# Kernel optimization log

Hardware: AMD Instinct MI355X
Metric: run time of the kernel (lower is better)

The kernel has to match this reference:

```python
import jax, jax.numpy as jnp
import numpy as np

H = 256        # hidden_dim
GD = 16        # genome_dim
GL = 16        # genome_len
L = 2          # n_layers
NH = 4         # n_heads
ED = 256       # embed_dim (of generated network)
CS = 256       # chunk_size (== H so chunk feedback into GRU is well-formed)
TOTAL = 4 * ED * ED + 4 * ED          # 263168
NCH = (TOTAL + CS - 1) // CS          # 1028 sequential GRU steps
B = 16


def setup_inputs() -> dict:
    key = jax.random.key(0)
    ks = iter(jax.random.split(key, 32))
    def p(shape, s=0.02):
        return jax.random.normal(next(ks), shape, jnp.float32) * s
    return dict(
        genome_seq=jax.random.normal(next(ks), (B, GL, GD), jnp.float32),
        embed_W=p((H, GD)), embed_b=jnp.zeros((H,), jnp.float32),
        qkv_W=p((L, 3 * H, H)), qkv_b=jnp.zeros((L, 3 * H), jnp.float32),
        attn_out_W=p((L, H, H)), attn_out_b=jnp.zeros((L, H), jnp.float32),
        ln1_g=jnp.ones((L, H), jnp.float32), ln1_b=jnp.zeros((L, H), jnp.float32),
        ln2_g=jnp.ones((L, H), jnp.float32), ln2_b=jnp.zeros((L, H), jnp.float32),
        ffn_W1=p((L, 4 * H, H)), ffn_b1=jnp.zeros((L, 4 * H), jnp.float32),
        ffn_W2=p((L, H, 4 * H)), ffn_b2=jnp.zeros((L, H), jnp.float32),
        gru_Wih=p((3 * H, H)), gru_Whh=p((3 * H, H)),
        gru_bih=jnp.zeros((3 * H,), jnp.float32), gru_bhh=jnp.zeros((3 * H,), jnp.float32),
        out_W=p((CS, H)), out_b=jnp.zeros((CS,), jnp.float32),
    )


def _ln(x, g, b, eps=1e-5):
    m = x.mean(-1, keepdims=True)
    v = ((x - m) ** 2).mean(-1, keepdims=True)
    return (x - m) / jnp.sqrt(v + eps) * g + b


def reference(genome_seq, embed_W, embed_b, qkv_W, qkv_b, attn_out_W, attn_out_b,
              ln1_g, ln1_b, ln2_g, ln2_b, ffn_W1, ffn_b1, ffn_W2, ffn_b2,
              gru_Wih, gru_Whh, gru_bih, gru_bhh, out_W, out_b):
    b = genome_seq.shape[0]
    dh = H // NH
    scale = 1.0 / np.sqrt(dh).astype(np.float32)

    h = genome_seq @ embed_W.T + embed_b                      # [B, S, H]
    # post-norm transformer encoder, relu FFN (PyTorch defaults, no dropout)
    for l in range(L):
        qkv = h @ qkv_W[l].T + qkv_b[l]                        # [B, S, 3H]
        q, k, v = jnp.split(qkv, 3, axis=-1)
        q = q.reshape(b, GL, NH, dh)
        k = k.reshape(b, GL, NH, dh)
        v = v.reshape(b, GL, NH, dh)
        scores = jnp.einsum('bshd,bthd->bhst', q, k) * scale
        attn = jax.nn.softmax(scores, axis=-1)
        o = jnp.einsum('bhst,bthd->bshd', attn, v).reshape(b, GL, H)
        h = _ln(h + o @ attn_out_W[l].T + attn_out_b[l], ln1_g[l], ln1_b[l])
        f = jax.nn.relu(h @ ffn_W1[l].T + ffn_b1[l]) @ ffn_W2[l].T + ffn_b2[l]
        h = _ln(h + f, ln2_g[l], ln2_b[l])

    latent = h.mean(axis=1)                                    # [B, H]

    # sequential chunk generation: 1 GRU step + Linear per chunk, fed back
    def step(carry, _):
        x, hid = carry
        gi = x @ gru_Wih.T + gru_bih
        gh = hid @ gru_Whh.T + gru_bhh
        ir, iz, inn = jnp.split(gi, 3, axis=-1)
        hr, hz, hn = jnp.split(gh, 3, axis=-1)
        r = jax.nn.sigmoid(ir + hr)
        z = jax.nn.sigmoid(iz + hz)
        n = jnp.tanh(inn + r * hn)
        hid = (1.0 - z) * n + z * hid
        chunk = hid @ out_W.T + out_b                          # [B, CS]
        return (chunk, hid), chunk

    h0 = jnp.zeros((b, H), latent.dtype)
    _, chunks = jax.lax.scan(step, (latent, h0), None, length=NCH)  # [NCH, B, CS]
    flat = jnp.moveaxis(chunks, 0, 1).reshape(b, NCH * CS)
    return flat[:, :TOTAL]
```

## Files before the change

### kernel.cpp

```cpp
#include <hip/hip_runtime.h>


typedef unsigned int uint_t;
typedef int v4i __attribute__((ext_vector_type(4)));

static constexpr size_t WS_HB   = 0;
static constexpr size_t WS_QKV  = 65536;
static constexpr size_t WS_AO   = 262144;
static constexpr size_t WS_F1   = 327680;
static constexpr size_t WS_LAT  = 589824;
static constexpr size_t WS_GI0  = 593920;
static constexpr size_t WS_CV   = 606208;
static constexpr size_t WS_MS   = 607232;
static constexpr size_t WS_M8   = 608256;
static constexpr size_t WS_HSEQ = 673792;

__device__ inline float sigf(float x){
    return __builtin_amdgcn_rcpf(1.0f + __builtin_amdgcn_exp2f(-1.442695041f*x));
}
__device__ inline float tanh_fast(float x){
    return 1.0f - 2.0f*__builtin_amdgcn_rcpf(1.0f + __builtin_amdgcn_exp2f(2.885390082f*x));
}


__global__ __launch_bounds__(256) void k_embed(const float* gs, const float* eW,
                                               const float* eb, float* ws){
    int bs = blockIdx.x;
    int i  = threadIdx.x;
    const float* g = gs + bs*16;
    float acc = eb[i];
#pragma unroll
    for(int d=0; d<16; ++d) acc += g[d]*eW[i*16+d];
    ws[WS_HB + (size_t)bs*256 + i] = acc;
}

__global__ __launch_bounds__(256) void k_qkv(const float* qkvW, const float* qkvb,
                                             float* ws, int l){
    __shared__ float hr[16][256];
    int b = blockIdx.x, jc = blockIdx.y;
    for(int idx=threadIdx.x; idx<4096; idx+=256)
        hr[idx>>8][idx&255] = ws[WS_HB + (size_t)(b*16+(idx>>8))*256 + (idx&255)];
    __syncthreads();
    int j = jc*256 + threadIdx.x;
    float bias = qkvb[l*768 + j];
    float acc[16];
#pragma unroll
    for(int s=0;s<16;++s) acc[s]=bias;
    const float* wr = qkvW + (size_t)(l*768 + j)*256;
    for(int k=0;k<256;k+=4){
        float4 w4 = *(const float4*)(wr+k);
#pragma unroll
        for(int s=0;s<16;++s)
            acc[s] += w4.x*hr[s][k] + w4.y*hr[s][k+1] + w4.z*hr[s][k+2] + w4.w*hr[s][k+3];
    }
    for(int s=0;s<16;++s) ws[WS_QKV + (size_t)(b*16+s)*768 + j] = acc[s];
}

__global__ __launch_bounds__(256) void k_attn(float* ws){
    __shared__ float ql[16][64], kl[16][64], vl[16][64], sc[16][16];
    int b = blockIdx.x>>2, hh = blockIdx.x&3;
    for(int idx=threadIdx.x; idx<1024; idx+=256){
        int s_=idx>>6, d=idx&63;
        const float* base = &ws[WS_QKV + (size_t)(b*16+s_)*768 + hh*64 + d];
        ql[s_][d]=base[0]; kl[s_][d]=base[256]; vl[s_][d]=base[512];
    }
    __syncthreads();
    int s = threadIdx.x>>4, t = threadIdx.x&15;
    float a=0.f;
#pragma unroll
    for(int d=0; d<64; ++d) a += ql[s][d]*kl[t][d];
    sc[s][t] = a*0.125f;
    __syncthreads();
    if(threadIdx.x<16){
        int r=threadIdx.x;
        float m=-1e30f;
#pragma unroll
        for(int tt=0;tt<16;++tt) m=fmaxf(m,sc[r][tt]);
        float e[16]; float sum=0.f;
#pragma unroll
        for(int tt=0;tt<16;++tt){ e[tt]=__expf(sc[r][tt]-m); sum+=e[tt]; }
        float inv=1.0f/sum;
#pragma unroll
        for(int tt=0;tt<16;++tt) sc[r][tt]=e[tt]*inv;
    }
    __syncthreads();
    int dg = (threadIdx.x&15)*4;
#pragma unroll
    for(int dd=0;dd<4;++dd){
        int d = dg+dd; float o=0.f;
#pragma unroll
        for(int tt=0;tt<16;++tt) o += sc[s][tt]*vl[tt][d];
        ws[WS_AO + (size_t)(b*16+s)*256 + hh*64 + d] = o;
    }
}

__global__ __launch_bounds__(256) void k_ao_ln(const float* aoW, const float* aob,
                                               const float* g1, const float* b1,
                                               float* ws, int l){
    __shared__ float ao[256]; __shared__ float red[256];
    int bs = blockIdx.x, i = threadIdx.x;
    ao[i] = ws[WS_AO + (size_t)bs*256 + i];
    __syncthreads();
    const float* wr = aoW + (size_t)(l*256+i)*256;
    float acc = aob[l*256+i];
    for(int k=0;k<256;k+=4){
        float4 w4 = *(const float4*)(wr+k);
        acc += w4.x*ao[k]+w4.y*ao[k+1]+w4.z*ao[k+2]+w4.w*ao[k+3];
    }
    float x = ws[WS_HB + (size_t)bs*256 + i] + acc;
    red[i]=x; __syncthreads();
    for(int off=128;off>0;off>>=1){ if(i<off) red[i]+=red[i+off]; __syncthreads(); }
    float m = red[0]*(1.0f/256.0f); __syncthreads();
    float d = x-m;
    red[i]=d*d; __syncthreads();
    for(int off=128;off>0;off>>=1){ if(i<off) red[i]+=red[i+off]; __syncthreads(); }
    float v = red[0]*(1.0f/256.0f);
    float y = d / sqrtf(v+1e-5f);
    ws[WS_HB + (size_t)bs*256 + i] = y*g1[l*256+i] + b1[l*256+i];
}

__global__ __launch_bounds__(256) void k_ffn1(const float* W1, const float* fb1,
                                              float* ws, int l){
    __shared__ float hr[16][256];
    int b = blockIdx.x, jc = blockIdx.y;
    for(int idx=threadIdx.x; idx<4096; idx+=256)
        hr[idx>>8][idx&255] = ws[WS_HB + (size_t)(b*16+(idx>>8))*256 + (idx&255)];
    __syncthreads();
    int j = jc*256 + threadIdx.x;
    float bias = fb1[l*1024+j];
    float acc[16];
#pragma unroll
    for(int s=0;s<16;++s) acc[s]=bias;
    const float* wr = W1 + (size_t)(l*1024+j)*256;
    for(int k=0;k<256;k+=4){
        float4 w4 = *(const float4*)(wr+k);
#pragma unroll
        for(int s=0;s<16;++s)
            acc[s] += w4.x*hr[s][k] + w4.y*hr[s][k+1] + w4.z*hr[s][k+2] + w4.w*hr[s][k+3];
    }
    for(int s=0;s<16;++s)
        ws[WS_F1 + (size_t)(b*16+s)*1024 + j] = fmaxf(acc[s],0.0f);
}

__global__ __launch_bounds__(256) void k_ffn2_ln(const float* W2, const float* fb2,
                                                 const float* g2, const float* b2v,
                                                 float* ws, int l){
    __shared__ float f1r[1024]; __shared__ float red[256];
    int bs = blockIdx.x, i = threadIdx.x;
    for(int idx=i; idx<1024; idx+=256) f1r[idx] = ws[WS_F1 + (size_t)bs*1024 + idx];
    __syncthreads();
    const float* wr = W2 + (size_t)(l*256+i)*1024;
    float acc = fb2[l*256+i];
    for(int k=0;k<1024;k+=4){
        float4 w4 = *(const float4*)(wr+k);
        acc += w4.x*f1r[k]+w4.y*f1r[k+1]+w4.z*f1r[k+2]+w4.w*f1r[k+3];
    }
    float x = ws[WS_HB + (size_t)bs*256 + i] + acc;
    red[i]=x; __syncthreads();
    for(int off=128;off>0;off>>=1){ if(i<off) red[i]+=red[i+off]; __syncthreads(); }
    float m = red[0]*(1.0f/256.0f); __syncthreads();
    float d = x-m;
    red[i]=d*d; __syncthreads();
    for(int off=128;off>0;off>>=1){ if(i<off) red[i]+=red[i+off]; __syncthreads(); }
    float v = red[0]*(1.0f/256.0f);
    float y = d / sqrtf(v+1e-5f);
    ws[WS_HB + (size_t)bs*256 + i] = y*g2[l*256+i] + b2v[l*256+i];
}

__global__ __launch_bounds__(256) void k_latent(float* ws){
    int b=blockIdx.x, i=threadIdx.x; float a=0.f;
#pragma unroll
    for(int s=0;s<16;++s) a += ws[WS_HB + (size_t)(b*16+s)*256 + i];
    ws[WS_LAT + (size_t)b*256 + i] = a*(1.0f/16.0f);
}


__global__ __launch_bounds__(768) void k_gi0(const float* Wih, const float* bih,
                                             float* ws){
    __shared__ float lat[256];
    int b=blockIdx.x, j=threadIdx.x;
    if(j<256) lat[j]=ws[WS_LAT + (size_t)b*256 + j];
    __syncthreads();
    const float* wr = Wih + (size_t)j*256;
    float acc = bih[j];
    for(int k=0;k<256;k+=4){
        float4 w4=*(const float4*)(wr+k);
        acc += w4.x*lat[k]+w4.y*lat[k+1]+w4.z*lat[k+2]+w4.w*lat[k+3];
    }
    ws[WS_GI0 + (size_t)b*768 + j] = acc;
}

__global__ __launch_bounds__(256) void k_prepm(const float* Wih, const float* Whh,
                                               const float* bih, const float* bhh,
                                               const float* outW, const float* outb,
                                               float* ws){
    __shared__ float wrow[256]; __shared__ float red[256];
    __shared__ signed char q8[256];
    int r=blockIdx.x, c=threadIdx.x;
    bool hasA = (r<768);
    wrow[c] = hasA ? Wih[(size_t)r*256+c] : 0.0f;
    __syncthreads();
    float m;
    if(hasA){
        float a=0.f;
        for(int k=0;k<256;++k) a += wrow[k]*outW[(size_t)k*256+c];
        if(r<512) a += Whh[(size_t)r*256+c];
        m=a;
    } else {
        m = Whh[(size_t)(r-256)*256+c];
    }
    red[c] = wrow[c]*outb[c];
    __syncthreads();
    for(int off=128;off>0;off>>=1){ if(c<off) red[c]+=red[c+off]; __syncthreads(); }
    if(c==0){
        float cv;
        if(r<512)       cv = red[0] + bih[r] + bhh[r];
        else if(r<768)  cv = red[0] + bih[r];
        else            cv = bhh[r-256];
        ws[WS_CV + r] = cv;
    }
    __syncthreads();
    red[c] = fabsf(m);
    __syncthreads();
    for(int off=128;off>0;off>>=1){ if(c<off) red[c]=fmaxf(red[c],red[c+off]); __syncthreads(); }
    float rowmax = red[0];
    float inv = rowmax>0.f ? 127.0f/rowmax : 0.0f;
    q8[c] = (signed char)__float2int_rn(m*inv);
    if(c==0) ws[WS_MS + r] = rowmax>0.f ? rowmax*(1.0f/(127.0f*127.0f)) : 0.0f;
    __syncthreads();
    if(c<64){
        uint_t u = ((uint_t)(unsigned char)q8[4*c  ])
                 | ((uint_t)(unsigned char)q8[4*c+1] << 8)
                 | ((uint_t)(unsigned char)q8[4*c+2] << 16)
                 | ((uint_t)(unsigned char)q8[4*c+3] << 24);
        ((uint_t*)ws)[WS_M8 + (size_t)r*64 + c] = u;
    }
}


__global__ __launch_bounds__(512,2) void k_chain(const float* bhh, float* ws){
    __shared__ alignas(16) signed char h8[2][256];
    int tid = threadIdx.x;
    int b   = blockIdx.x;
    int l   = tid & 63;
    int w   = tid >> 6;
    int col = l & 15;
    int grp = l >> 4;
    int g0  = w*32 + col;

    const uint_t* Mdw = (const uint_t*)ws + WS_M8;

    v4i wf[8][4];
    float C8[8], MS8[8];
#pragma unroll
    for(int s=0;s<4;++s){
#pragma unroll
        for(int half=0; half<2; ++half){
            int f = s*2 + half;
            int row = s*256 + w*32 + half*16 + col;
            const uint_t* src = Mdw + (size_t)row*64 + grp*4;
#pragma unroll
            for(int kt=0;kt<4;++kt)
                wf[f][kt] = *(const v4i*)(src + kt*16);
            C8[f]  = ws[WS_CV + row];
            MS8[f] = ws[WS_MS + row];
        }
    }

    const float* gi = ws + WS_GI0 + (size_t)b*768;
    int g1 = g0 + 16;
    float r0 = sigf(gi[g0]     + bhh[g0]);
    float z0 = sigf(gi[256+g0] + bhh[256+g0]);
    float n0 = tanh_fast(gi[512+g0] + r0*bhh[512+g0]);
    float hp0 = (1.0f-z0)*n0;
    float r1 = sigf(gi[g1]     + bhh[g1]);
    float z1 = sigf(gi[256+g1] + bhh[256+g1]);
    float n1 = tanh_fast(gi[512+g1] + r1*bhh[512+g1]);
    float hp1 = (1.0f-z1)*n1;

    float* hsp = ws + WS_HSEQ + (size_t)b*256;
    if(grp < 2){
        float v = grp ? hp1 : hp0;
        h8[0][w*32 + (l&31)] = (signed char)__float2int_rn(v*127.0f);
        hsp[w*32 + (l&31)] = v;
    }
    asm volatile("s_waitcnt lgkmcnt(0)" ::: "memory");
    __builtin_amdgcn_s_barrier();
    asm volatile("" ::: "memory");

    const v4i vzero = {0,0,0,0};
    int po = 0;
    for(int t=1; t<1028; ++t){
        hsp += 4096;
        v4i af[4];
#pragma unroll
        for(int kt=0;kt<4;++kt)
            af[kt] = *(const v4i*)&h8[po][kt*64 + grp*16];
        v4i acc[8];
#pragma unroll
        for(int f=0;f<8;++f){
            acc[f] = __builtin_amdgcn_mfma_i32_16x16x64_i8(af[0], wf[f][0], vzero, 0,0,0);
#pragma unroll
            for(int kt=1;kt<4;++kt)
                acc[f] = __builtin_amdgcn_mfma_i32_16x16x64_i8(af[kt], wf[f][kt], acc[f], 0,0,0);
        }
        float yr0 = MS8[0]*(float)acc[0][0] + C8[0];
        float yr1 = MS8[1]*(float)acc[1][0] + C8[1];
        float yz0 = MS8[2]*(float)acc[2][0] + C8[2];
        float yz1 = MS8[3]*(float)acc[3][0] + C8[3];
        float yn0 = MS8[4]*(float)acc[4][0] + C8[4];
        float yn1 = MS8[5]*(float)acc[5][0] + C8[5];
        float yh0 = MS8[6]*(float)acc[6][0] + C8[6];
        float yh1 = MS8[7]*(float)acc[7][0] + C8[7];
        float rr0 = sigf(yr0), rr1 = sigf(yr1);
        float zz0 = sigf(yz0), zz1 = sigf(yz1);
        float nn0 = tanh_fast(yn0 + rr0*yh0);
        float nn1 = tanh_fast(yn1 + rr1*yh1);
        hp0 = (1.0f-zz0)*nn0 + zz0*hp0;
        hp1 = (1.0f-zz1)*nn1 + zz1*hp1;
        if(grp < 2){
            float v = grp ? hp1 : hp0;
            h8[po^1][w*32 + (l&31)] = (signed char)__float2int_rn(v*127.0f);
            hsp[w*32 + (l&31)] = v;
        }
        asm volatile("s_waitcnt lgkmcnt(0)" ::: "memory");
        __builtin_amdgcn_s_barrier();
        asm volatile("" ::: "memory");
        po ^= 1;
    }
}

__global__ __launch_bounds__(256) void k_epi(const float* outW, const float* outb,
                                             const float* ws, float* out){
    __shared__ float ht[16][256];
    int t = blockIdx.x, j = threadIdx.x;
    for(int idx=j; idx<4096; idx+=256)
        ht[idx>>8][idx&255] = ws[WS_HSEQ + (size_t)t*4096 + idx];
    __syncthreads();
    const float* wr = outW + (size_t)j*256;
    float bias = outb[j];
    float acc[16];
#pragma unroll
    for(int bb=0;bb<16;++bb) acc[bb]=bias;
    for(int k=0;k<256;k+=4){
        float4 w4 = *(const float4*)(wr+k);
#pragma unroll
        for(int bb=0;bb<16;++bb)
            acc[bb] += w4.x*ht[bb][k]+w4.y*ht[bb][k+1]+w4.z*ht[bb][k+2]+w4.w*ht[bb][k+3];
    }
#pragma unroll
    for(int bb=0;bb<16;++bb)
        out[(size_t)bb*263168 + (size_t)t*256 + j] = acc[bb];
}


extern "C" void kernel_launch(void* const* d_in, const int* in_sizes, int n_in,
                              void* d_out, int out_size, void* d_ws, size_t ws_size,
                              hipStream_t stream){
    const float* gs   = (const float*)d_in[0];
    const float* eW   = (const float*)d_in[1];
    const float* eb   = (const float*)d_in[2];
    const float* qkvW = (const float*)d_in[3];
    const float* qkvb = (const float*)d_in[4];
    const float* aoW  = (const float*)d_in[5];
    const float* aob  = (const float*)d_in[6];
    const float* g1   = (const float*)d_in[7];
    const float* b1   = (const float*)d_in[8];
    const float* g2   = (const float*)d_in[9];
    const float* b2   = (const float*)d_in[10];
    const float* W1   = (const float*)d_in[11];
    const float* fb1  = (const float*)d_in[12];
    const float* W2   = (const float*)d_in[13];
    const float* fb2  = (const float*)d_in[14];
    const float* Wih  = (const float*)d_in[15];
    const float* Whh  = (const float*)d_in[16];
    const float* bih  = (const float*)d_in[17];
    const float* bhh  = (const float*)d_in[18];
    const float* outW = (const float*)d_in[19];
    const float* outb = (const float*)d_in[20];
    float* ws  = (float*)d_ws;
    float* out = (float*)d_out;

    k_embed<<<256,256,0,stream>>>(gs,eW,eb,ws);
    for(int l=0;l<2;++l){
        k_qkv    <<<dim3(16,3),256,0,stream>>>(qkvW,qkvb,ws,l);
        k_attn   <<<64,256,0,stream>>>(ws);
        k_ao_ln  <<<256,256,0,stream>>>(aoW,aob,g1,b1,ws,l);
        k_ffn1   <<<dim3(16,4),256,0,stream>>>(W1,fb1,ws,l);
        k_ffn2_ln<<<256,256,0,stream>>>(W2,fb2,g2,b2,ws,l);
    }
    k_latent<<<16,256,0,stream>>>(ws);
    k_gi0   <<<16,768,0,stream>>>(Wih,bih,ws);
    k_prepm <<<1024,256,0,stream>>>(Wih,Whh,bih,bhh,outW,outb,ws);
    k_chain <<<16,512,0,stream>>>(bhh,ws);
    k_epi   <<<1028,256,0,stream>>>(outW,outb,ws,out);
}
```

Before: 1.127 ms.

## Fuse transformer stages into fewer kernels and halve per-lane GRU gate work

Merges embedding with the weight-prep kernel, fuses QKV projection with attention per batch-head, and fuses attention-out, LayerNorm, FFN1 and FFN2 with a second LayerNorm into one kernel per token. The latent mean is also folded into the gi0 kernel. Together this cuts the launch count from about 16 to 7 and removes intermediate global round-trips. In the GRU chain kernel each lane now handles one hidden unit, picked by lane parity, instead of computing two and discarding one, which shortens the serial per-step gate math. The cost is that the fused FFN kernel has every one of 256 blocks re-read the full W1 matrix, with less parallelism per weight row.

Result: faster. 1.096 ms (-2.7%).

```diff
diff --git a/kernel.cpp b/kernel.cpp
--- a/kernel.cpp
+++ b/kernel.cpp
@@ -5,10 +5,7 @@
 typedef int v4i __attribute__((ext_vector_type(4)));
 
 static constexpr size_t WS_HB   = 0;
-static constexpr size_t WS_QKV  = 65536;
 static constexpr size_t WS_AO   = 262144;
-static constexpr size_t WS_F1   = 327680;
-static constexpr size_t WS_LAT  = 589824;
 static constexpr size_t WS_GI0  = 593920;
 static constexpr size_t WS_CV   = 606208;
 static constexpr size_t WS_MS   = 607232;
@@ -23,180 +20,26 @@
 }
 
 
-__global__ __launch_bounds__(256) void k_embed(const float* gs, const float* eW,
-                                               const float* eb, float* ws){
-    int bs = blockIdx.x;
-    int i  = threadIdx.x;
-    const float* g = gs + bs*16;
-    float acc = eb[i];
-#pragma unroll
-    for(int d=0; d<16; ++d) acc += g[d]*eW[i*16+d];
-    ws[WS_HB + (size_t)bs*256 + i] = acc;
-}
-
-__global__ __launch_bounds__(256) void k_qkv(const float* qkvW, const float* qkvb,
-                                             float* ws, int l){
-    __shared__ float hr[16][256];
-    int b = blockIdx.x, jc = blockIdx.y;
-    for(int idx=threadIdx.x; idx<4096; idx+=256)
-        hr[idx>>8][idx&255] = ws[WS_HB + (size_t)(b*16+(idx>>8))*256 + (idx&255)];
-    __syncthreads();
-    int j = jc*256 + threadIdx.x;
-    float bias = qkvb[l*768 + j];
-    float acc[16];
-#pragma unroll
-    for(int s=0;s<16;++s) acc[s]=bias;
-    const float* wr = qkvW + (size_t)(l*768 + j)*256;
-    for(int k=0;k<256;k+=4){
-        float4 w4 = *(const float4*)(wr+k);
-#pragma unroll
-        for(int s=0;s<16;++s)
-            acc[s] += w4.x*hr[s][k] + w4.y*hr[s][k+1] + w4.z*hr[s][k+2] + w4.w*hr[s][k+3];
-    }
-    for(int s=0;s<16;++s) ws[WS_QKV + (size_t)(b*16+s)*768 + j] = acc[s];
-}
-
-__global__ __launch_bounds__(256) void k_attn(float* ws){
-    __shared__ float ql[16][64], kl[16][64], vl[16][64], sc[16][16];
-    int b = blockIdx.x>>2, hh = blockIdx.x&3;
-    for(int idx=threadIdx.x; idx<1024; idx+=256){
-        int s_=idx>>6, d=idx&63;
-        const float* base = &ws[WS_QKV + (size_t)(b*16+s_)*768 + hh*64 + d];
-        ql[s_][d]=base[0]; kl[s_][d]=base[256]; vl[s_][d]=base[512];
-    }
-    __syncthreads();
-    int s = threadIdx.x>>4, t = threadIdx.x&15;
-    float a=0.f;
-#pragma unroll
-    for(int d=0; d<64; ++d) a += ql[s][d]*kl[t][d];
-    sc[s][t] = a*0.125f;
-    __syncthreads();
-    if(threadIdx.x<16){
-        int r=threadIdx.x;
-        float m=-1e30f;
-#pragma unroll
-        for(int tt=0;tt<16;++tt) m=fmaxf(m,sc[r][tt]);
-        float e[16]; float sum=0.f;
-#pragma unroll
-        for(int tt=0;tt<16;++tt){ e[tt]=__expf(sc[r][tt]-m); sum+=e[tt]; }
-        float inv=1.0f/sum;
-#pragma unroll
-        for(int tt=0;tt<16;++tt) sc[r][tt]=e[tt]*inv;
-    }
-    __syncthreads();
-    int dg = (threadIdx.x&15)*4;
-#pragma unroll
-    for(int dd=0;dd<4;++dd){
-        int d = dg+dd; float o=0.f;
-#pragma unroll
-        for(int tt=0;tt<16;++tt) o += sc[s][tt]*vl[tt][d];
-        ws[WS_AO + (size_t)(b*16+s)*256 + hh*64 + d] = o;
-    }
-}
-
-__global__ __launch_bounds__(256) void k_ao_ln(const float* aoW, const float* aob,
-                                               const float* g1, const float* b1,
-                                               float* ws, int l){
-    __shared__ float ao[256]; __shared__ float red[256];
-    int bs = blockIdx.x, i = threadIdx.x;
-    ao[i] = ws[WS_AO + (size_t)bs*256 + i];
-    __syncthreads();
-    const float* wr = aoW + (size_t)(l*256+i)*256;
-    float acc = aob[l*256+i];
-    for(int k=0;k<256;k+=4){
-        float4 w4 = *(const float4*)(wr+k);
-        acc += w4.x*ao[k]+w4.y*ao[k+1]+w4.z*ao[k+2]+w4.w*ao[k+3];
-    }
-    float x = ws[WS_HB + (size_t)bs*256 + i] + acc;
-    red[i]=x; __syncthreads();
-    for(int off=128;off>0;off>>=1){ if(i<off) red[i]+=red[i+off]; __syncthreads(); }
-    float m = red[0]*(1.0f/256.0f); __syncthreads();
-    float d = x-m;
-    red[i]=d*d; __syncthreads();
-    for(int off=128;off>0;off>>=1){ if(i<off) red[i]+=red[i+off]; __syncthreads(); }
-    float v = red[0]*(1.0f/256.0f);
-    float y = d / sqrtf(v+1e-5f);
-    ws[WS_HB + (size_t)bs*256 + i] = y*g1[l*256+i] + b1[l*256+i];
-}
-
-__global__ __launch_bounds__(256) void k_ffn1(const float* W1, const float* fb1,
-                                              float* ws, int l){
-    __shared__ float hr[16][256];
-    int b = blockIdx.x, jc = blockIdx.y;
-    for(int idx=threadIdx.x; idx<4096; idx+=256)
-        hr[idx>>8][idx&255] = ws[WS_HB + (size_t)(b*16+(idx>>8))*256 + (idx&255)];
-    __syncthreads();
-    int j = jc*256 + threadIdx.x;
-    float bias = fb1[l*1024+j];
-    float acc[16];
-#pragma unroll
-    for(int s=0;s<16;++s) acc[s]=bias;
-    const float* wr = W1 + (size_t)(l*1024+j)*256;
-    for(int k=0;k<256;k+=4){
-        float4 w4 = *(const float4*)(wr+k);
-#pragma unroll
-        for(int s=0;s<16;++s)
-            acc[s] += w4.x*hr[s][k] + w4.y*hr[s][k+1] + w4.z*hr[s][k+2] + w4.w*hr[s][k+3];
-    }
-    for(int s=0;s<16;++s)
-        ws[WS_F1 + (size_t)(b*16+s)*1024 + j] = fmaxf(acc[s],0.0f);
-}
-
-__global__ __launch_bounds__(256) void k_ffn2_ln(const float* W2, const float* fb2,
-                                                 const float* g2, const float* b2v,
-                                                 float* ws, int l){
-    __shared__ float f1r[1024]; __shared__ float red[256];
-    int bs = blockIdx.x, i = threadIdx.x;
-    for(int idx=i; idx<1024; idx+=256) f1r[idx] = ws[WS_F1 + (size_t)bs*1024 + idx];
-    __syncthreads();
-    const float* wr = W2 + (size_t)(l*256+i)*1024;
-    float acc = fb2[l*256+i];
-    for(int k=0;k<1024;k+=4){
-        float4 w4 = *(const float4*)(wr+k);
-        acc += w4.x*f1r[k]+w4.y*f1r[k+1]+w4.z*f1r[k+2]+w4.w*f1r[k+3];
-    }
-    float x = ws[WS_HB + (size_t)bs*256 + i] + acc;
-    red[i]=x; __syncthreads();
-    for(int off=128;off>0;off>>=1){ if(i<off) red[i]+=red[i+off]; __syncthreads(); }
-    float m = red[0]*(1.0f/256.0f); __syncthreads();
-    float d = x-m;
-    red[i]=d*d; __syncthreads();
-    for(int off=128;off>0;off>>=1){ if(i<off) red[i]+=red[i+off]; __syncthreads(); }
-    float v = red[0]*(1.0f/256.0f);
-    float y = d / sqrtf(v+1e-5f);
-    ws[WS_HB + (size_t)bs*256 + i] = y*g2[l*256+i] + b2v[l*256+i];
-}
-
-__global__ __launch_bounds__(256) void k_latent(float* ws){
-    int b=blockIdx.x, i=threadIdx.x; float a=0.f;
-#pragma unroll
-    for(int s=0;s<16;++s) a += ws[WS_HB + (size_t)(b*16+s)*256 + i];
-    ws[WS_LAT + (size_t)b*256 + i] = a*(1.0f/16.0f);
-}
-
-
-__global__ __launch_bounds__(768) void k_gi0(const float* Wih, const float* bih,
-                                             float* ws){
-    __shared__ float lat[256];
-    int b=blockIdx.x, j=threadIdx.x;
-    if(j<256) lat[j]=ws[WS_LAT + (size_t)b*256 + j];
-    __syncthreads();
-    const float* wr = Wih + (size_t)j*256;
-    float acc = bih[j];
-    for(int k=0;k<256;k+=4){
-        float4 w4=*(const float4*)(wr+k);
-        acc += w4.x*lat[k]+w4.y*lat[k+1]+w4.z*lat[k+2]+w4.w*lat[k+3];
-    }
-    ws[WS_GI0 + (size_t)b*768 + j] = acc;
-}
-
-__global__ __launch_bounds__(256) void k_prepm(const float* Wih, const float* Whh,
-                                               const float* bih, const float* bhh,
-                                               const float* outW, const float* outb,
-                                               float* ws){
+__global__ __launch_bounds__(256) void k_emb_prep(
+    const float* gs, const float* eW, const float* eb,
+    const float* Wih, const float* Whh, const float* bih, const float* bhh,
+    const float* outW, const float* outb, float* ws)
+{
     __shared__ float wrow[256]; __shared__ float red[256];
     __shared__ signed char q8[256];
-    int r=blockIdx.x, c=threadIdx.x;
+
+    if(blockIdx.x < 256){
+        int bs = blockIdx.x;
+        int i  = threadIdx.x;
+        const float* g = gs + bs*16;
+        float acc = eb[i];
+#pragma unroll
+        for(int d=0; d<16; ++d) acc += g[d]*eW[i*16+d];
+        ws[WS_HB + (size_t)bs*256 + i] = acc;
+        return;
+    }
+
+    int r = blockIdx.x - 256, c = threadIdx.x;
     bool hasA = (r<768);
     wrow[c] = hasA ? Wih[(size_t)r*256+c] : 0.0f;
     __syncthreads();
@@ -238,6 +81,161 @@
 }
 
 
+__global__ __launch_bounds__(256) void k_qkv_attn(const float* qkvW, const float* qkvb,
+                                                  float* ws, int l){
+    __shared__ float s_h[16][256];
+    __shared__ float s_q[16][64], s_k[16][64], s_v[16][64];
+    __shared__ float s_sc[16][16];
+    int b = blockIdx.x>>2, hh = blockIdx.x&3;
+    int tid = threadIdx.x;
+
+    for(int u=tid; u<4096; u+=256)
+        s_h[u>>8][u&255] = ws[WS_HB + (size_t)(b*16+(u>>8))*256 + (u&255)];
+    __syncthreads();
+
+    if(tid<192){
+        int p = tid>>6, d = tid&63;
+        int row = l*768 + p*256 + hh*64 + d;
+        const float* wr = qkvW + (size_t)row*256;
+        float bias = qkvb[row];
+        float acc[16];
+#pragma unroll
+        for(int s=0;s<16;++s) acc[s]=bias;
+        for(int k=0;k<256;k+=4){
+            float4 w4 = *(const float4*)(wr+k);
+#pragma unroll
+            for(int s=0;s<16;++s){
+                float4 h4 = *(const float4*)&s_h[s][k];
+                acc[s] += w4.x*h4.x + w4.y*h4.y + w4.z*h4.z + w4.w*h4.w;
+            }
+        }
+        float (*dst)[64] = (p==0) ? s_q : (p==1) ? s_k : s_v;
+#pragma unroll
+        for(int s=0;s<16;++s) dst[s][d] = acc[s];
+    }
+    __syncthreads();
+
+    {
+        int s = tid>>4, t = tid&15;
+        float a=0.f;
+#pragma unroll
+        for(int d=0; d<64; ++d) a += s_q[s][d]*s_k[t][d];
+        s_sc[s][t] = a*0.125f;
+    }
+    __syncthreads();
+    if(tid<16){
+        int r=tid;
+        float m=-1e30f;
+#pragma unroll
+        for(int tt=0;tt<16;++tt) m=fmaxf(m,s_sc[r][tt]);
+        float e[16]; float sum=0.f;
+#pragma unroll
+        for(int tt=0;tt<16;++tt){ e[tt]=__expf(s_sc[r][tt]-m); sum+=e[tt]; }
+        float inv=1.0f/sum;
+#pragma unroll
+        for(int tt=0;tt<16;++tt) s_sc[r][tt]=e[tt]*inv;
+    }
+    __syncthreads();
+    for(int u=tid; u<1024; u+=256){
+        int s=u>>6, d=u&63;
+        float o=0.f;
+#pragma unroll
+        for(int t2=0;t2<16;++t2) o += s_sc[s][t2]*s_v[t2][d];
+        ws[WS_AO + (size_t)(b*16+s)*256 + hh*64 + d] = o;
+    }
+}
+
+
+__global__ __launch_bounds__(256) void k_ao_ffn(
+    const float* aoW, const float* aob, const float* g1, const float* b1,
+    const float* W1, const float* fb1, const float* W2, const float* fb2,
+    const float* g2, const float* b2v, float* ws, int l)
+{
+    __shared__ float s_x[256];
+    __shared__ float s_f1[1024];
+    __shared__ float red[256];
+    int bs = blockIdx.x, i = threadIdx.x;
+
+    s_x[i] = ws[WS_AO + (size_t)bs*256 + i];
+    float hb = ws[WS_HB + (size_t)bs*256 + i];
+    __syncthreads();
+
+    const float* wr = aoW + (size_t)(l*256+i)*256;
+    float acc = aob[l*256+i];
+    for(int k=0;k<256;k+=4){
+        float4 w4 = *(const float4*)(wr+k);
+        float4 h4 = *(const float4*)&s_x[k];
+        acc += w4.x*h4.x + w4.y*h4.y + w4.z*h4.z + w4.w*h4.w;
+    }
+    float x = hb + acc;
+    red[i]=x; __syncthreads();
+    for(int off=128;off>0;off>>=1){ if(i<off) red[i]+=red[i+off]; __syncthreads(); }
+    float mn = red[0]*(1.0f/256.0f); __syncthreads();
+    float d = x-mn;
+    red[i]=d*d; __syncthreads();
+    for(int off=128;off>0;off>>=1){ if(i<off) red[i]+=red[i+off]; __syncthreads(); }
+    float vv = red[0]*(1.0f/256.0f);
+    float h1 = (d / sqrtf(vv+1e-5f))*g1[l*256+i] + b1[l*256+i];
+    __syncthreads();
+    s_x[i] = h1;
+    __syncthreads();
+
+#pragma unroll
+    for(int jj=0;jj<4;++jj){
+        int j = jj*256 + i;
+        const float* w1r = W1 + (size_t)(l*1024+j)*256;
+        float a1 = fb1[l*1024+j];
+        for(int k=0;k<256;k+=4){
+            float4 w4 = *(const float4*)(w1r+k);
+            float4 h4 = *(const float4*)&s_x[k];
+            a1 += w4.x*h4.x + w4.y*h4.y + w4.z*h4.z + w4.w*h4.w;
+        }
+        s_f1[j] = fmaxf(a1, 0.0f);
+    }
+    __syncthreads();
+
+    const float* w2r = W2 + (size_t)(l*256+i)*1024;
+    float a2 = fb2[l*256+i];
+    for(int k=0;k<1024;k+=4){
+        float4 w4 = *(const float4*)(w2r+k);
+        float4 h4 = *(const float4*)&s_f1[k];
+        a2 += w4.x*h4.x + w4.y*h4.y + w4.z*h4.z + w4.w*h4.w;
+    }
+    float x2 = h1 + a2;
+    red[i]=x2; __syncthreads();
+    for(int off=128;off>0;off>>=1){ if(i<off) red[i]+=red[i+off]; __syncthreads(); }
+    float mn2 = red[0]*(1.0f/256.0f); __syncthreads();
+    float d2 = x2-mn2;
+    red[i]=d2*d2; __syncthreads();
+    for(int off=128;off>0;off>>=1){ if(i<off) red[i]+=red[i+off]; __syncthreads(); }
+    float vv2 = red[0]*(1.0f/256.0f);
+    float y2 = d2 / sqrtf(vv2+1e-5f);
+    ws[WS_HB + (size_t)bs*256 + i] = y2*g2[l*256+i] + b2v[l*256+i];
+}
+
+
+__global__ __launch_bounds__(768) void k_lat_gi0(const float* Wih, const float* bih,
+                                                 float* ws){
+    __shared__ float lat[256];
+    int b=blockIdx.x, j=threadIdx.x;
+    if(j<256){
+        float a=0.f;
+#pragma unroll
+        for(int s=0;s<16;++s) a += ws[WS_HB + (size_t)(b*16+s)*256 + j];
+        lat[j] = a*(1.0f/16.0f);
+    }
+    __syncthreads();
+    const float* wr = Wih + (size_t)j*256;
+    float acc = bih[j];
+    for(int k=0;k<256;k+=4){
+        float4 w4=*(const float4*)(wr+k);
+        float4 l4=*(const float4*)&lat[k];
+        acc += w4.x*l4.x + w4.y*l4.y + w4.z*l4.z + w4.w*l4.w;
+    }
+    ws[WS_GI0 + (size_t)b*768 + j] = acc;
+}
+
+
 __global__ __launch_bounds__(512,2) void k_chain(const float* bhh, float* ws){
     __shared__ alignas(16) signed char h8[2][256];
     int tid = threadIdx.x;
@@ -246,12 +244,12 @@
     int w   = tid >> 6;
     int col = l & 15;
     int grp = l >> 4;
-    int g0  = w*32 + col;
+    int par = grp & 1;
+    int ge  = w*32 + par*16 + col;
 
     const uint_t* Mdw = (const uint_t*)ws + WS_M8;
 
     v4i wf[8][4];
-    float C8[8], MS8[8];
 #pragma unroll
     for(int s=0;s<4;++s){
 #pragma unroll
@@ -262,27 +260,26 @@
 #pragma unroll
             for(int kt=0;kt<4;++kt)
                 wf[f][kt] = *(const v4i*)(src + kt*16);
-            C8[f]  = ws[WS_CV + row];
-            MS8[f] = ws[WS_MS + row];
-        }
+        }
+    }
+    float Cs[4], MSs[4];
+#pragma unroll
+    for(int s=0;s<4;++s){
+        int row = s*256 + ge;
+        Cs[s]  = ws[WS_CV + row];
+        MSs[s] = ws[WS_MS + row];
     }
 
     const float* gi = ws + WS_GI0 + (size_t)b*768;
-    int g1 = g0 + 16;
-    float r0 = sigf(gi[g0]     + bhh[g0]);
-    float z0 = sigf(gi[256+g0] + bhh[256+g0]);
-    float n0 = tanh_fast(gi[512+g0] + r0*bhh[512+g0]);
-    float hp0 = (1.0f-z0)*n0;
-    float r1 = sigf(gi[g1]     + bhh[g1]);
-    float z1 = sigf(gi[256+g1] + bhh[256+g1]);
-    float n1 = tanh_fast(gi[512+g1] + r1*bhh[512+g1]);
-    float hp1 = (1.0f-z1)*n1;
+    float r0 = sigf(gi[ge]     + bhh[ge]);
+    float z0 = sigf(gi[256+ge] + bhh[256+ge]);
+    float n0 = tanh_fast(gi[512+ge] + r0*bhh[512+ge]);
+    float hp = (1.0f-z0)*n0;
 
     float* hsp = ws + WS_HSEQ + (size_t)b*256;
     if(grp < 2){
-        float v = grp ? hp1 : hp0;
-        h8[0][w*32 + (l&31)] = (signed char)__float2int_rn(v*127.0f);
-        hsp[w*32 + (l&31)] = v;
+        h8[0][w*32 + (l&31)] = (signed char)__float2int_rn(hp*127.0f);
+        hsp[w*32 + (l&31)] = hp;
     }
     asm volatile("s_waitcnt lgkmcnt(0)" ::: "memory");
     __builtin_amdgcn_s_barrier();
@@ -304,24 +301,21 @@
             for(int kt=1;kt<4;++kt)
                 acc[f] = __builtin_amdgcn_mfma_i32_16x16x64_i8(af[kt], wf[f][kt], acc[f], 0,0,0);
         }
-        float yr0 = MS8[0]*(float)acc[0][0] + C8[0];
-        float yr1 = MS8[1]*(float)acc[1][0] + C8[1];
-        float yz0 = MS8[2]*(float)acc[2][0] + C8[2];
-        float yz1 = MS8[3]*(float)acc[3][0] + C8[3];
-        float yn0 = MS8[4]*(float)acc[4][0] + C8[4];
-        float yn1 = MS8[5]*(float)acc[5][0] + C8[5];
-        float yh0 = MS8[6]*(float)acc[6][0] + C8[6];
-        float yh1 = MS8[7]*(float)acc[7][0] + C8[7];
-        float rr0 = sigf(yr0), rr1 = sigf(yr1);
-        float zz0 = sigf(yz0), zz1 = sigf(yz1);
-        float nn0 = tanh_fast(yn0 + rr0*yh0);
-        float nn1 = tanh_fast(yn1 + rr1*yh1);
-        hp0 = (1.0f-zz0)*nn0 + zz0*hp0;
-        hp1 = (1.0f-zz1)*nn1 + zz1*hp1;
+        int a_r = par ? acc[1][0] : acc[0][0];
+        int a_z = par ? acc[3][0] : acc[2][0];
+        int a_n = par ? acc[5][0] : acc[4][0];
+        int a_h = par ? acc[7][0] : acc[6][0];
+        float yr = MSs[0]*(float)a_r + Cs[0];
+        float yz = MSs[1]*(float)a_z + Cs[1];
+        float yn = MSs[2]*(float)a_n + Cs[2];
+        float yh = MSs[3]*(float)a_h + Cs[3];
+        float rr = sigf(yr);
+        float zz = sigf(yz);
+        float nn = tanh_fast(yn + rr*yh);
+        hp = (1.0f-zz)*nn + zz*hp;
         if(grp < 2){
-            float v = grp ? hp1 : hp0;
-            h8[po^1][w*32 + (l&31)] = (signed char)__float2int_rn(v*127.0f);
-            hsp[w*32 + (l&31)] = v;
+            h8[po^1][w*32 + (l&31)] = (signed char)__float2int_rn(hp*127.0f);
+            hsp[w*32 + (l&31)] = hp;
         }
         asm volatile("s_waitcnt lgkmcnt(0)" ::: "memory");
         __builtin_amdgcn_s_barrier();
@@ -381,17 +375,12 @@
     float* ws  = (float*)d_ws;
     float* out = (float*)d_out;
 
-    k_embed<<<256,256,0,stream>>>(gs,eW,eb,ws);
+    k_emb_prep<<<1280,256,0,stream>>>(gs,eW,eb,Wih,Whh,bih,bhh,outW,outb,ws);
     for(int l=0;l<2;++l){
-        k_qkv    <<<dim3(16,3),256,0,stream>>>(qkvW,qkvb,ws,l);
-        k_attn   <<<64,256,0,stream>>>(ws);
-        k_ao_ln  <<<256,256,0,stream>>>(aoW,aob,g1,b1,ws,l);
-        k_ffn1   <<<dim3(16,4),256,0,stream>>>(W1,fb1,ws,l);
-        k_ffn2_ln<<<256,256,0,stream>>>(W2,fb2,g2,b2,ws,l);
-    }
-    k_latent<<<16,256,0,stream>>>(ws);
-    k_gi0   <<<16,768,0,stream>>>(Wih,bih,ws);
-    k_prepm <<<1024,256,0,stream>>>(Wih,Whh,bih,bhh,outW,outb,ws);
-    k_chain <<<16,512,0,stream>>>(bhh,ws);
-    k_epi   <<<1028,256,0,stream>>>(outW,outb,ws,out);
-}
+        k_qkv_attn<<<64,256,0,stream>>>(qkvW,qkvb,ws,l);
+        k_ao_ffn  <<<256,256,0,stream>>>(aoW,aob,g1,b1,W1,fb1,W2,fb2,g2,b2,ws,l);
+    }
+    k_lat_gi0<<<16,768,0,stream>>>(Wih,bih,ws);
+    k_chain  <<<16,512,0,stream>>>(bhh,ws);
+    k_epi    <<<1028,256,0,stream>>>(outW,outb,ws,out);
+}
```
